# Kernel optimization log

Hardware: AMD Instinct MI355X
Metric: run time of the kernel (lower is better)

The kernel has to match this reference:

```python
import jax, jax.numpy as jnp
import numpy as np


def _layernorm(x, g, b, eps=1e-5):
    mu = jnp.mean(x, axis=-1, keepdims=True)
    xc = x - mu
    var = jnp.mean(xc * xc, axis=-1, keepdims=True)
    return xc * jax.lax.rsqrt(var + eps) * g + b


def _s5(u, Lambda_re, Lambda_im, B_re, B_im, C_re, C_im, Dskip, log_step):
    # Diagonal complex SSM with ZOH discretization (S5).
    Lam = Lambda_re + 1j * Lambda_im                       # (P,) complex64
    Lam_bar = jnp.exp(Lam * jnp.exp(log_step))             # (P,)
    B_bar = ((Lam_bar - 1.0) / Lam)[:, None] * (B_re + 1j * B_im)  # (P, D)
    Bu = jnp.einsum('bld,pd->blp', u.astype(jnp.complex64), B_bar)  # (B, L, P)
    A = jnp.broadcast_to(Lam_bar, Bu.shape)

    def combine(e1, e2):
        a1, b1 = e1
        a2, b2 = e2
        return a1 * a2, a2 * b1 + b2

    _, xs = jax.lax.associative_scan(combine, (A, Bu), axis=1)  # parallel scan over L
    y = 2.0 * jnp.real(jnp.einsum('blp,dp->bld', xs, C_re + 1j * C_im))
    return y + Dskip * u


def setup_inputs() -> dict:
    key = jax.random.key(0)
    ks = jax.random.split(key, 10)
    B, L, D, P = 4, 2048, 1024, 64
    F = int(D * 2.0)  # ff_mult = 2.0
    x = jax.random.normal(ks[0], (B, L, D), jnp.float32)
    ln1_g = jnp.ones((D,), jnp.float32)
    ln1_b = jnp.zeros((D,), jnp.float32)
    ln2_g = jnp.ones((D,), jnp.float32)
    ln2_b = jnp.zeros((D,), jnp.float32)
    Lambda_re = -(0.5 + jax.random.uniform(ks[1], (P,), jnp.float32))  # stable poles
    Lambda_im = jnp.pi * jnp.arange(P, dtype=jnp.float32)              # HiPPO-like spread
    B_re = jax.random.normal(ks[2], (P, D), jnp.float32) / np.float32(np.sqrt(D))
    B_im = jax.random.normal(ks[3], (P, D), jnp.float32) / np.float32(np.sqrt(D))
    C_re = jax.random.normal(ks[4], (D, P), jnp.float32) / np.float32(np.sqrt(P))
    C_im = jax.random.normal(ks[5], (D, P), jnp.float32) / np.float32(np.sqrt(P))
    Dskip = jax.random.normal(ks[6], (D,), jnp.float32)
    dt_min, dt_max = 1e-3, 1e-1
    log_step = (np.float32(np.log(dt_min))
                + jax.random.uniform(ks[7], (P,), jnp.float32)
                * np.float32(np.log(dt_max) - np.log(dt_min)))
    W_enc = jax.random.normal(ks[8], (2 * F, D), jnp.float32) / np.float32(np.sqrt(D))
    W_dec = jax.random.normal(ks[9], (D, F), jnp.float32) / np.float32(np.sqrt(F))
    return dict(x=x, ln1_g=ln1_g, ln1_b=ln1_b, ln2_g=ln2_g, ln2_b=ln2_b,
                Lambda_re=Lambda_re, Lambda_im=Lambda_im, B_re=B_re, B_im=B_im,
                C_re=C_re, C_im=C_im, Dskip=Dskip, log_step=log_step,
                W_enc=W_enc, W_dec=W_dec)


def reference(x, ln1_g, ln1_b, ln2_g, ln2_b, Lambda_re, Lambda_im, B_re, B_im,
              C_re, C_im, Dskip, log_step, W_enc, W_dec):
    # S5Block: pre-LN -> S5 -> GELU -> residual (dropout = identity in eval)
    fx = _layernorm(x, ln1_g, ln1_b)
    h = jax.nn.gelu(_s5(fx, Lambda_re, Lambda_im, B_re, B_im, C_re, C_im, Dskip, log_step),
                    approximate=False) + fx
    # pre-LN GEGLU feed-forward -> residual
    fx2 = _layernorm(h, ln2_g, ln2_b)
    e = fx2 @ W_enc.T                      # (B, L, 2F)
    a, gate = jnp.split(e, 2, axis=-1)
    e = a * jax.nn.gelu(gate, approximate=False)
    return e @ W_dec.T + fx2
```

## Files before the change

kernel.cpp:

```cpp
#include <hip/hip_runtime.h>
#include <hip/hip_bf16.h>
#include <math.h>

typedef unsigned short u16;
typedef __bf16 v8bf __attribute__((ext_vector_type(8)));
typedef float f32x4 __attribute__((ext_vector_type(4)));
typedef float f32x16 __attribute__((ext_vector_type(16)));

__device__ __forceinline__ float us2f(u16 h) {
    union { unsigned int u; float f; } v; v.u = ((unsigned int)h) << 16; return v.f;
}
__device__ __forceinline__ u16 f2us(float f) {
    union { float f; unsigned int u; } v; v.f = f;
    unsigned int r = v.u + 0x7fffu + ((v.u >> 16) & 1u);
    return (u16)(r >> 16);
}
__device__ __forceinline__ float gelu_f(float x) {
    return 0.5f * x * (1.0f + erff(x * 0.70710678118654752f));
}
__device__ __forceinline__ void gload_lds16(const u16* g, u16* l) {
    auto gp = reinterpret_cast<const __attribute__((address_space(1))) unsigned int*>(
        (uintptr_t)g);
    auto lp = reinterpret_cast<__attribute__((address_space(3))) unsigned int*>(
        (uintptr_t)l);
    __builtin_amdgcn_global_load_lds(gp, lp, 16, 0, 0);
}

__global__ __launch_bounds__(256) void prepall_kernel(
    const float* __restrict__ Wenc, u16* __restrict__ WeB,
    const float* __restrict__ Wdec, u16* __restrict__ WdB,
    const float* __restrict__ Lre, const float* __restrict__ Lim,
    const float* __restrict__ lstep,
    const float* __restrict__ Bre, const float* __restrict__ Bim,
    const float* __restrict__ Cre, const float* __restrict__ Cim,
    u16* __restrict__ Bbar, u16* __restrict__ C2)
{
    const int b = blockIdx.x, tid = threadIdx.x;
    if (b < 3072) {
        const float* in = (b < 2048) ? Wenc : Wdec;
        u16* outp = (b < 2048) ? WeB : WdB;
        const int i = (b < 2048 ? b : b - 2048) * 2048 + tid * 8;
        float4 a = *reinterpret_cast<const float4*>(in + i);
        float4 c = *reinterpret_cast<const float4*>(in + i + 4);
        u16 o[8] = { f2us(a.x), f2us(a.y), f2us(a.z), f2us(a.w),
                     f2us(c.x), f2us(c.y), f2us(c.z), f2us(c.w) };
        *reinterpret_cast<uint4*>(outp + i) = *reinterpret_cast<uint4*>(o);
        return;
    }
    const int idx = (b - 3072) * 256 + tid;
    if (idx < 65536) {
        const int p = idx >> 10, d = idx & 1023;
        const float lr = Lre[p], li = Lim[p];
        const float dt = expf(lstep[p]);
        const float er = expf(lr * dt);
        const float ar = er * cosf(li * dt), ai = er * sinf(li * dt);
        const float nr = ar - 1.0f, ni = ai;
        const float den = lr * lr + li * li;
        const float cr = (nr * lr + ni * li) / den;
        const float ci = (ni * lr - nr * li) / den;
        const float br = Bre[idx], bi = Bim[idx];
        Bbar[p * 1024 + d]        = f2us(cr * br - ci * bi);
        Bbar[(64 + p) * 1024 + d] = f2us(cr * bi + ci * br);
    } else {
        const int i = idx - 65536;
        const int d = i >> 6, p = i & 63;
        C2[d * 128 + p]      = f2us( 2.0f * Cre[i]);
        C2[d * 128 + 64 + p] = f2us(-2.0f * Cim[i]);
    }
}

template<typename TIN>
__global__ __launch_bounds__(256) void ln_kernel(const TIN* __restrict__ in,
                                                 const float* __restrict__ g,
                                                 const float* __restrict__ b,
                                                 u16* __restrict__ out)
{
    const int row = blockIdx.x, tid = threadIdx.x;
    const size_t base = (size_t)row * 1024 + tid * 4;
    float x0, x1, x2, x3;
    if constexpr (sizeof(TIN) == 4) {
        float4 v = *reinterpret_cast<const float4*>(in + base);
        x0 = v.x; x1 = v.y; x2 = v.z; x3 = v.w;
    } else {
        ushort4 v = *reinterpret_cast<const ushort4*>((const u16*)in + base);
        x0 = us2f(v.x); x1 = us2f(v.y); x2 = us2f(v.z); x3 = us2f(v.w);
    }
    float s = x0 + x1 + x2 + x3;
    float q = x0*x0 + x1*x1 + x2*x2 + x3*x3;
    #pragma unroll
    for (int o = 32; o; o >>= 1) { s += __shfl_down(s, o); q += __shfl_down(q, o); }
    __shared__ float red[8];
    if ((tid & 63) == 0) { red[tid >> 6] = s; red[4 + (tid >> 6)] = q; }
    __syncthreads();
    s = red[0] + red[1] + red[2] + red[3];
    q = red[4] + red[5] + red[6] + red[7];
    const float mu = s * (1.0f / 1024.0f);
    const float rs = rsqrtf(q * (1.0f / 1024.0f) - mu * mu + 1e-5f);
    float4 gv = *reinterpret_cast<const float4*>(g + tid * 4);
    float4 bv = *reinterpret_cast<const float4*>(b + tid * 4);
    ushort4 o4;
    o4.x = f2us((x0 - mu) * rs * gv.x + bv.x);
    o4.y = f2us((x1 - mu) * rs * gv.y + bv.y);
    o4.z = f2us((x2 - mu) * rs * gv.z + bv.z);
    o4.w = f2us((x3 - mu) * rs * gv.w + bv.w);
    *reinterpret_cast<ushort4*>(out + base) = o4;
}

__global__ __launch_bounds__(256) void scan_kernel(
    const float* __restrict__ Bu,
    const float* __restrict__ Lre, const float* __restrict__ Lim,
    const float* __restrict__ lstep,
    u16* __restrict__ A2)
{
    const int b = blockIdx.x >> 6;
    const int p = blockIdx.x & 63;
    const int t = threadIdx.x;
    const float lr = Lre[p], li = Lim[p];
    const float dt = expf(lstep[p]);
    const float er = expf(lr * dt);
    const float ar = er * cosf(li * dt), ai = er * sinf(li * dt);

    const size_t base = ((size_t)b * 2048 + t * 8) * 128;
    float xr[8], xi[8];
    float sr = 0.f, si = 0.f;
    #pragma unroll
    for (int i = 0; i < 8; ++i) {
        const float br = Bu[base + i * 128 + p];
        const float bi = Bu[base + i * 128 + 64 + p];
        const float nr = ar * sr - ai * si + br;
        const float ni = ar * si + ai * sr + bi;
        sr = nr; si = ni;
        xr[i] = sr; xi[i] = si;
    }
    float fr = ar, fi = ai;
    #pragma unroll
    for (int s = 0; s < 3; ++s) { const float t2 = fr*fr - fi*fi; fi = 2.f*fr*fi; fr = t2; }
    __shared__ float Er[256], Ei[256];
    Er[t] = sr; Ei[t] = si;
    __syncthreads();
    float vr = sr, vi = si;
    for (int off = 1; off < 256; off <<= 1) {
        float pr = 0.f, pi = 0.f;
        if (t >= off) { pr = Er[t - off]; pi = Ei[t - off]; }
        __syncthreads();
        vr += fr * pr - fi * pi;
        vi += fr * pi + fi * pr;
        Er[t] = vr; Ei[t] = vi;
        const float nf = fr*fr - fi*fi; fi = 2.f*fr*fi; fr = nf;
        __syncthreads();
    }
    float cr = 0.f, ci = 0.f;
    if (t > 0) { cr = Er[t - 1]; ci = Ei[t - 1]; }
    float gr = ar * cr - ai * ci, gi = ar * ci + ai * cr;
    #pragma unroll
    for (int i = 0; i < 8; ++i) {
        xr[i] += gr; xi[i] += gi;
        const float n2 = ar * gr - ai * gi; gi = ar * gi + ai * gr; gr = n2;
    }
    #pragma unroll
    for (int i = 0; i < 8; ++i) {
        const size_t m = (size_t)b * 2048 + t * 8 + i;
        A2[m * 128 + p]      = f2us(xr[i]);
        A2[m * 128 + 64 + p] = f2us(xi[i]);
    }
}

template<int BM, int BN>
__global__ __launch_bounds__(64) void gemm_small_kernel(
    const u16* __restrict__ A, const u16* __restrict__ B, float* __restrict__ Cout,
    const int N, const int K)
{
    __shared__ u16 lsA[BM * 32];
    __shared__ u16 lsB[BN * 32];
    const int tid = threadIdx.x;
    const int lane = tid & 63;
    const int m0 = blockIdx.y * BM, n0 = blockIdx.x * BN;
    f32x4 acc[4][4] = {};
    for (int k0 = 0; k0 < K; k0 += 32) {
        #pragma unroll
        for (int j = 0; j < 4; ++j) {
            const int s = j * 64 + tid;
            gload_lds16(A + (size_t)(m0 + (s >> 2)) * K + k0 + (s & 3) * 8,
                        lsA + (s - lane) * 8);
            gload_lds16(B + (size_t)(n0 + (s >> 2)) * K + k0 + (s & 3) * 8,
                        lsB + (s - lane) * 8);
        }
        __syncthreads();
        v8bf af[4], bfv[4];
        #pragma unroll
        for (int f = 0; f < 4; ++f)
            af[f] = *reinterpret_cast<const v8bf*>(
                lsA + (f * 16 + (lane & 15)) * 32 + (lane >> 4) * 8);
        #pragma unroll
        for (int f = 0; f < 4; ++f)
            bfv[f] = *reinterpret_cast<const v8bf*>(
                lsB + (f * 16 + (lane & 15)) * 32 + (lane >> 4) * 8);
        #pragma unroll
        for (int fm = 0; fm < 4; ++fm)
            #pragma unroll
            for (int fn = 0; fn < 4; ++fn)
                acc[fm][fn] = __builtin_amdgcn_mfma_f32_16x16x32_bf16(
                    af[fm], bfv[fn], acc[fm][fn], 0, 0, 0);
        __syncthreads();
    }
    #pragma unroll
    for (int fm = 0; fm < 4; ++fm)
    #pragma unroll
    for (int fn = 0; fn < 4; ++fn)
    #pragma unroll
    for (int i = 0; i < 4; ++i) {
        const int r = m0 + fm * 16 + (lane >> 4) * 4 + i;
        const int c = n0 + fn * 16 + (lane & 15);
        Cout[(size_t)r * N + c] = acc[fm][fn][i];
    }
}

#define BARM()   asm volatile("s_barrier" ::: "memory")
#define LGKM0()  asm volatile("s_waitcnt lgkmcnt(0)" ::: "memory")
#define VMK(n)   asm volatile("s_waitcnt vmcnt(" #n ")" ::: "memory")
#define PRIO1    __builtin_amdgcn_s_setprio(1)
#define PRIO0    __builtin_amdgcn_s_setprio(0)
#define MMA32(acc, a, b) \
    acc = __builtin_amdgcn_mfma_f32_32x32x16_bf16(a, b, acc, 0, 0, 0)
#define RDA(mf, kk) (*reinterpret_cast<const v8bf*>( \
    cb + ((wm) * 128 + (mf) * 32 + l31) * 64 + ((((kk) * 2 + lh) ^ l7) * 8)))
#define RDBG(ag, kk) (*reinterpret_cast<const v8bf*>( \
    cb + (256 + (ag) * 128 + (wn) * 32 + l31) * 64 + ((((kk) * 2 + lh) ^ l7) * 8)))
#define RDB4(kk) (*reinterpret_cast<const v8bf*>( \
    cb + (256 + (wn) * 32 + l31) * 64 + ((((kk) * 2 + lh) ^ l7) * 8)))
#define STAGE(s, bi) do { \
    u16* d0_ = lds + (bi) * BUFE + ((s) * 128 + (wid * 2 + 0) * 8) * 64; \
    u16* d1_ = lds + (bi) * BUFE + ((s) * 128 + (wid * 2 + 1) * 8) * 64; \
    gload_lds16(pS[s][0], d0_); gload_lds16(pS[s][1], d1_); \
    pS[s][0] += 64; pS[s][1] += 64; } while (0)

#define GLU_HB(cb_, ab_, bb_, stA_, stB_) do { \
    const u16* cb = (cb_); \
    v8bf bfA[4], bfG[4], af[4]; \
    _Pragma("unroll") for (int mf = 0; mf < 4; ++mf) af[mf] = RDA(mf, 0); \
    _Pragma("unroll") for (int kk = 0; kk < 4; ++kk) { \
        bfA[kk] = RDBG(0, kk); bfG[kk] = RDBG(1, kk); } \
    if (stA_) STAGE(0, ab_); \
    PRIO1; \
    _Pragma("unroll") for (int mf = 0; mf < 4; ++mf) { \
        MMA32(accA[mf], af[mf], bfA[0]); MMA32(accG[mf], af[mf], bfG[0]); } \
    PRIO0; LGKM0(); BARM(); \
    _Pragma("unroll") for (int mf = 0; mf < 4; ++mf) af[mf] = RDA(mf, 1); \
    if (stA_) STAGE(1, ab_); \
    PRIO1; \
    _Pragma("unroll") for (int mf = 0; mf < 4; ++mf) { \
        MMA32(accA[mf], af[mf], bfA[1]); MMA32(accG[mf], af[mf], bfG[1]); } \
    PRIO0; LGKM0(); BARM(); \
    _Pragma("unroll") for (int mf = 0; mf < 4; ++mf) af[mf] = RDA(mf, 2); \
    if (stB_) STAGE(2, bb_); \
    PRIO1; \
    _Pragma("unroll") for (int mf = 0; mf < 4; ++mf) { \
        MMA32(accA[mf], af[mf], bfA[2]); MMA32(accG[mf], af[mf], bfG[2]); } \
    PRIO0; LGKM0(); BARM(); \
    _Pragma("unroll") for (int mf = 0; mf < 4; ++mf) af[mf] = RDA(mf, 3); \
    if (stB_) STAGE(3, bb_); \
    PRIO1; \
    _Pragma("unroll") for (int mf = 0; mf < 4; ++mf) { \
        MMA32(accA[mf], af[mf], bfA[3]); MMA32(accG[mf], af[mf], bfG[3]); } \
    PRIO0; LGKM0(); \
    if (stB_) { VMK(4); } else { VMK(0); } \
    BARM(); } while (0)

template<int NBX>
__global__ __launch_bounds__(512, 2) void geglu8p_kernel(
    const u16* __restrict__ A, const u16* __restrict__ Bm, u16* __restrict__ Cout,
    const int K, const int NO, const int NT)
{
    constexpr int BUFE = 512 * 64;
    __shared__ u16 lds[2 * BUFE];
    const int tid = threadIdx.x, lane = tid & 63, wid = tid >> 6;
    const int wm = wid >> 2, wn = wid & 3;
    const int l31 = lane & 31, lh = lane >> 5, l7 = lane & 7;
    const int bid = blockIdx.x;
    const int swz = (bid & 7) * (NBX * 4) + (bid >> 3);
    const int by = swz / NBX, bx = swz % NBX;
    const int m0 = by * 256, n0 = bx * 128;

    const int rl = lane >> 3;
    const int scol = ((lane & 7) ^ rl) * 8;
    const u16* pS[4][2];
    #pragma unroll
    for (int j = 0; j < 2; ++j) {
        const int rloc = (wid * 2 + j) * 8 + rl;
        pS[0][j] = A  + (size_t)(m0 + rloc)       * K + scol;
        pS[1][j] = A  + (size_t)(m0 + 128 + rloc) * K + scol;
        pS[2][j] = Bm + (size_t)(n0 + rloc)       * K + scol;
        pS[3][j] = Bm + (size_t)(NO + n0 + rloc)  * K + scol;
    }

    f32x16 accA[4] = {};
    f32x16 accG[4] = {};

    #pragma unroll
    for (int t = 0; t < 2; ++t) { STAGE(0, t); STAGE(1, t); STAGE(2, t); STAGE(3, t); }
    VMK(0);
    BARM();

    const int NI = NT >> 1;
    for (int i = 0; i < NI; ++i) {
        const bool s1 = (i > 0);
        const bool s2 = (2 * i + 2 < NT);
        const bool s3 = (2 * i + 3 < NT);
        GLU_HB(lds,        1, 0, s1, s2);
        GLU_HB(lds + BUFE, 0, 1, s2, s3);
    }

    #pragma unroll
    for (int mf = 0; mf < 4; ++mf)
    #pragma unroll
    for (int q = 0; q < 16; ++q) {
        const int r = m0 + wm * 128 + mf * 32 + (q & 3) + 8 * (q >> 2) + 4 * lh;
        const int c = n0 + wn * 32 + l31;
        Cout[(size_t)r * NO + c] = f2us(accA[mf][q] * gelu_f(accG[mf][q]));
    }
}

#define P4_HB(cb_, ab_, bb_, stA_, stB_) do { \
    const u16* cb = (cb_); \
    v8bf bfv[4], af0[4], af1[4]; \
    _Pragma("unroll") for (int mf = 0; mf < 4; ++mf) { \
        af0[mf] = RDA(mf, 0); af1[mf] = RDA(mf, 1); } \
    _Pragma("unroll") for (int kk = 0; kk < 4; ++kk) bfv[kk] = RDB4(kk); \
    if (stA_) { STAGE(0, ab_); STAGE(1, ab_); } \
    PRIO1; \
    _Pragma("unroll") for (int mf = 0; mf < 4; ++mf) { \
        MMA32(acc[mf], af0[mf], bfv[0]); MMA32(acc[mf], af1[mf], bfv[1]); } \
    PRIO0; LGKM0(); BARM(); \
    _Pragma("unroll") for (int mf = 0; mf < 4; ++mf) { \
        af0[mf] = RDA(mf, 2); af1[mf] = RDA(mf, 3); } \
    if (stB_) STAGE(2, bb_); \
    PRIO1; \
    _Pragma("unroll") for (int mf = 0; mf < 4; ++mf) { \
        MMA32(acc[mf], af0[mf], bfv[2]); MMA32(acc[mf], af1[mf], bfv[3]); } \
    PRIO0; LGKM0(); \
    if (stB_) { VMK(2); } else { VMK(0); } \
    BARM(); } while (0)

template<int EPI, int NBX>
__global__ __launch_bounds__(512, 2) void gemm4p_kernel(
    const u16* __restrict__ A, const u16* __restrict__ Bm, void* __restrict__ Cout,
    const int K, const int NO, const int NT,
    const u16* __restrict__ aux, const float* __restrict__ dskip)
{
    constexpr int BUFE = 384 * 64;
    __shared__ u16 lds[2 * BUFE];
    const int tid = threadIdx.x, lane = tid & 63, wid = tid >> 6;
    const int wm = wid >> 2, wn = wid & 3;
    const int l31 = lane & 31, lh = lane >> 5, l7 = lane & 7;
    const int bid = blockIdx.x;
    const int swz = (bid & 7) * (NBX * 4) + (bid >> 3);
    const int by = swz / NBX, bx = swz % NBX;
    const int m0 = by * 256, n0 = bx * 128;

    const int rl = lane >> 3;
    const int scol = ((lane & 7) ^ rl) * 8;
    const u16* pS[3][2];
    #pragma unroll
    for (int j = 0; j < 2; ++j) {
        const int rloc = (wid * 2 + j) * 8 + rl;
        pS[0][j] = A  + (size_t)(m0 + rloc)       * K + scol;
        pS[1][j] = A  + (size_t)(m0 + 128 + rloc) * K + scol;
        pS[2][j] = Bm + (size_t)(n0 + rloc)       * K + scol;
    }

    f32x16 acc[4] = {};

    #pragma unroll
    for (int t = 0; t < 2; ++t) { STAGE(0, t); STAGE(1, t); STAGE(2, t); }
    VMK(0);
    BARM();

    const int NI = NT >> 1;
    for (int i = 0; i < NI; ++i) {
        const bool s1 = (i > 0);
        const bool s2 = (2 * i + 2 < NT);
        const bool s3 = (2 * i + 3 < NT);
        P4_HB(lds,        1, 0, s1, s2);
        P4_HB(lds + BUFE, 0, 1, s2, s3);
    }

    #pragma unroll
    for (int mf = 0; mf < 4; ++mf)
    #pragma unroll
    for (int q = 0; q < 16; ++q) {
        const int r = m0 + wm * 128 + mf * 32 + (q & 3) + 8 * (q >> 2) + 4 * lh;
        const int c = n0 + wn * 32 + l31;
        const size_t o = (size_t)r * NO + c;
        const float v = acc[mf][q];
        if constexpr (EPI == 1) {
            const float u = us2f(aux[o]);
            const float t2 = v + dskip[c] * u;
            ((u16*)Cout)[o] = f2us(gelu_f(t2) + u);
        } else {
            ((float*)Cout)[o] = v + us2f(aux[o]);
        }
    }
}

static constexpr size_t OFF_FX  = 0;
static constexpr size_t OFF_BU  = 16777216;
static constexpr size_t OFF_A2  = 20971520;
static constexpr size_t OFF_E2  = 0;
static constexpr size_t OFF_FX2 = 33554432;
static constexpr size_t OFF_BB  = 50331648;
static constexpr size_t OFF_C2  = 50593792;
static constexpr size_t OFF_WE  = 50855936;
static constexpr size_t OFF_WD  = 59244544;

extern "C" void kernel_launch(void* const* d_in, const int* in_sizes, int n_in,
                              void* d_out, int out_size, void* d_ws, size_t ws_size,
                              hipStream_t stream) {
    const float* x    = (const float*)d_in[0];
    const float* l1g  = (const float*)d_in[1];
    const float* l1b  = (const float*)d_in[2];
    const float* l2g  = (const float*)d_in[3];
    const float* l2b  = (const float*)d_in[4];
    const float* Lre  = (const float*)d_in[5];
    const float* Lim  = (const float*)d_in[6];
    const float* Bre  = (const float*)d_in[7];
    const float* Bim  = (const float*)d_in[8];
    const float* Cre  = (const float*)d_in[9];
    const float* Cim  = (const float*)d_in[10];
    const float* Dsk  = (const float*)d_in[11];
    const float* lst  = (const float*)d_in[12];
    const float* Wenc = (const float*)d_in[13];
    const float* Wdec = (const float*)d_in[14];
    float* out = (float*)d_out;

    char* ws = (char*)d_ws;
    u16*   fx   = (u16*)(ws + OFF_FX);
    float* Bu   = (float*)(ws + OFF_BU);
    u16*   A2   = (u16*)(ws + OFF_A2);
    u16*   e2   = (u16*)(ws + OFF_E2);
    u16*   fx2  = (u16*)(ws + OFF_FX2);
    u16*   Bbar = (u16*)(ws + OFF_BB);
    u16*   C2   = (u16*)(ws + OFF_C2);
    u16*   WeB  = (u16*)(ws + OFF_WE);
    u16*   WdB  = (u16*)(ws + OFF_WD);
    u16*   h    = (u16*)d_out;

    ln_kernel<float><<<8192, 256, 0, stream>>>(x, l1g, l1b, fx);
    prepall_kernel<<<3584, 256, 0, stream>>>(Wenc, WeB, Wdec, WdB,
                                             Lre, Lim, lst, Bre, Bim, Cre, Cim,
                                             Bbar, C2);
    gemm_small_kernel<64, 64><<<dim3(2, 128), 64, 0, stream>>>(
        fx, Bbar, Bu, 128, 1024);
    scan_kernel<<<256, 256, 0, stream>>>(Bu, Lre, Lim, lst, A2);
    gemm4p_kernel<1, 8><<<256, 512, 0, stream>>>(
        A2, C2, h, 128, 1024, 2, fx, Dsk);
    ln_kernel<u16><<<8192, 256, 0, stream>>>(h, l2g, l2b, fx2);
    geglu8p_kernel<16><<<512, 512, 0, stream>>>(fx2, WeB, e2, 1024, 2048, 16);
    gemm4p_kernel<3, 8><<<256, 512, 0, stream>>>(
        e2, WdB, out, 2048, 1024, 32, fx2, nullptr);

    (void)in_sizes; (void)n_in; (void)out_size; (void)ws_size;
}
```

Before: 230.4 us.

## Retile down/C-projection GEMMs to 128x128 with 256-thread blocks, precompute LDS pointers

The 4-pass GEMM kernel (used for the S5 C-projection and the GEGLU down projection) moves from 256x128 tiles with 512 threads to 128x128 tiles with 256 threads and a 2x2 warp grid, each warp computing 64x64. The grid doubles to 512 blocks to improve CU occupancy and load balance. The GEGLU kernel keeps its tiling but gets a new LDS layout with A and B regions separated and per-lane LDS read pointers precomputed, which cuts address arithmetic. Smaller tiles lower per-block reuse and raise total global traffic, in exchange for more parallelism.

```diff
diff --git a/kernel.cpp b/kernel.cpp
--- a/kernel.cpp
+++ b/kernel.cpp
@@ -222,62 +222,51 @@
 #define PRIO0    __builtin_amdgcn_s_setprio(0)
 #define MMA32(acc, a, b) \
     acc = __builtin_amdgcn_mfma_f32_32x32x16_bf16(a, b, acc, 0, 0, 0)
-#define RDA(mf, kk) (*reinterpret_cast<const v8bf*>( \
-    cb + ((wm) * 128 + (mf) * 32 + l31) * 64 + ((((kk) * 2 + lh) ^ l7) * 8)))
-#define RDBG(ag, kk) (*reinterpret_cast<const v8bf*>( \
-    cb + (256 + (ag) * 128 + (wn) * 32 + l31) * 64 + ((((kk) * 2 + lh) ^ l7) * 8)))
-#define RDB4(kk) (*reinterpret_cast<const v8bf*>( \
-    cb + (256 + (wn) * 32 + l31) * 64 + ((((kk) * 2 + lh) ^ l7) * 8)))
-#define STAGE(s, bi) do { \
-    u16* d0_ = lds + (bi) * BUFE + ((s) * 128 + (wid * 2 + 0) * 8) * 64; \
-    u16* d1_ = lds + (bi) * BUFE + ((s) * 128 + (wid * 2 + 1) * 8) * 64; \
-    gload_lds16(pS[s][0], d0_); gload_lds16(pS[s][1], d1_); \
+
+#define G_RA(af, kk, BI) { _Pragma("unroll") \
+    for (int mf = 0; mf < 4; ++mf) \
+        af[mf] = *reinterpret_cast<const v8bf*>(pA[kk] + mf * 2048 + (BI) * 16384); }
+#define G_RB(kk, ag, BI) \
+    (*reinterpret_cast<const v8bf*>(pB[kk] + (ag) * 8192 + (BI) * 16384))
+#define G_ST(s, bi) do { \
+    const int db_ = (((s) & 2) ? 32768 : 0) + (bi) * 16384 + (((s) & 1) ? 8192 : 0); \
+    gload_lds16(pS[s][0], lds + db_ + (wid * 2 + 0) * 512); \
+    gload_lds16(pS[s][1], lds + db_ + (wid * 2 + 1) * 512); \
     pS[s][0] += 64; pS[s][1] += 64; } while (0)
-
-#define GLU_HB(cb_, ab_, bb_, stA_, stB_) do { \
-    const u16* cb = (cb_); \
-    v8bf bfA[4], bfG[4], af[4]; \
-    _Pragma("unroll") for (int mf = 0; mf < 4; ++mf) af[mf] = RDA(mf, 0); \
+#define G_MM(kk) { _Pragma("unroll") \
+    for (int mf = 0; mf < 4; ++mf) { \
+        MMA32(accA[mf], af[mf], bA[kk]); MMA32(accG[mf], af[mf], bG[kk]); } }
+#define G_TILE(BI, stA_, stB_) do { \
+    v8bf af[4], bA[4], bG[4]; \
+    G_RA(af, 0, BI); \
     _Pragma("unroll") for (int kk = 0; kk < 4; ++kk) { \
-        bfA[kk] = RDBG(0, kk); bfG[kk] = RDBG(1, kk); } \
-    if (stA_) STAGE(0, ab_); \
-    PRIO1; \
-    _Pragma("unroll") for (int mf = 0; mf < 4; ++mf) { \
-        MMA32(accA[mf], af[mf], bfA[0]); MMA32(accG[mf], af[mf], bfG[0]); } \
-    PRIO0; LGKM0(); BARM(); \
-    _Pragma("unroll") for (int mf = 0; mf < 4; ++mf) af[mf] = RDA(mf, 1); \
-    if (stA_) STAGE(1, ab_); \
-    PRIO1; \
-    _Pragma("unroll") for (int mf = 0; mf < 4; ++mf) { \
-        MMA32(accA[mf], af[mf], bfA[1]); MMA32(accG[mf], af[mf], bfG[1]); } \
-    PRIO0; LGKM0(); BARM(); \
-    _Pragma("unroll") for (int mf = 0; mf < 4; ++mf) af[mf] = RDA(mf, 2); \
-    if (stB_) STAGE(2, bb_); \
-    PRIO1; \
-    _Pragma("unroll") for (int mf = 0; mf < 4; ++mf) { \
-        MMA32(accA[mf], af[mf], bfA[2]); MMA32(accG[mf], af[mf], bfG[2]); } \
-    PRIO0; LGKM0(); BARM(); \
-    _Pragma("unroll") for (int mf = 0; mf < 4; ++mf) af[mf] = RDA(mf, 3); \
-    if (stB_) STAGE(3, bb_); \
-    PRIO1; \
-    _Pragma("unroll") for (int mf = 0; mf < 4; ++mf) { \
-        MMA32(accA[mf], af[mf], bfA[3]); MMA32(accG[mf], af[mf], bfG[3]); } \
-    PRIO0; LGKM0(); \
+        bA[kk] = G_RB(kk, 0, BI); bG[kk] = G_RB(kk, 1, BI); } \
+    if (stA_) G_ST(0, (BI) ^ 1); \
+    PRIO1; G_MM(0); PRIO0; LGKM0(); BARM(); \
+    G_RA(af, 1, BI); \
+    if (stA_) G_ST(1, (BI) ^ 1); \
+    PRIO1; G_MM(1); PRIO0; LGKM0(); BARM(); \
+    G_RA(af, 2, BI); \
+    if (stB_) G_ST(2, BI); \
+    PRIO1; G_MM(2); PRIO0; LGKM0(); BARM(); \
+    G_RA(af, 3, BI); \
+    if (stB_) G_ST(3, BI); \
+    PRIO1; G_MM(3); PRIO0; LGKM0(); \
     if (stB_) { VMK(4); } else { VMK(0); } \
     BARM(); } while (0)
 
 template<int NBX>
-__global__ __launch_bounds__(512, 2) void geglu8p_kernel(
+__global__ __launch_bounds__(512, 2) void geglu_kernel(
     const u16* __restrict__ A, const u16* __restrict__ Bm, u16* __restrict__ Cout,
     const int K, const int NO, const int NT)
 {
-    constexpr int BUFE = 512 * 64;
-    __shared__ u16 lds[2 * BUFE];
+    __shared__ u16 lds[65536];
     const int tid = threadIdx.x, lane = tid & 63, wid = tid >> 6;
     const int wm = wid >> 2, wn = wid & 3;
     const int l31 = lane & 31, lh = lane >> 5, l7 = lane & 7;
     const int bid = blockIdx.x;
-    const int swz = (bid & 7) * (NBX * 4) + (bid >> 3);
+    const int chunk = (int)gridDim.x >> 3;
+    const int swz = (bid & 7) * chunk + (bid >> 3);
     const int by = swz / NBX, bx = swz % NBX;
     const int m0 = by * 256, n0 = bx * 128;
 
@@ -292,12 +281,20 @@
         pS[2][j] = Bm + (size_t)(n0 + rloc)       * K + scol;
         pS[3][j] = Bm + (size_t)(NO + n0 + rloc)  * K + scol;
     }
+    const u16* pA[4];
+    const u16* pB[4];
+    #pragma unroll
+    for (int kk = 0; kk < 4; ++kk) {
+        const int phys = ((kk * 2 + lh) ^ l7) * 8;
+        pA[kk] = lds + (wm * 128 + l31) * 64 + phys;
+        pB[kk] = lds + 32768 + (wn * 32 + l31) * 64 + phys;
+    }
 
     f32x16 accA[4] = {};
     f32x16 accG[4] = {};
 
     #pragma unroll
-    for (int t = 0; t < 2; ++t) { STAGE(0, t); STAGE(1, t); STAGE(2, t); STAGE(3, t); }
+    for (int t = 0; t < 2; ++t) { G_ST(0, t); G_ST(1, t); G_ST(2, t); G_ST(3, t); }
     VMK(0);
     BARM();
 
@@ -306,8 +303,8 @@
         const bool s1 = (i > 0);
         const bool s2 = (2 * i + 2 < NT);
         const bool s3 = (2 * i + 3 < NT);
-        GLU_HB(lds,        1, 0, s1, s2);
-        GLU_HB(lds + BUFE, 0, 1, s2, s3);
+        G_TILE(0, s1, s2);
+        G_TILE(1, s2, s3);
     }
 
     #pragma unroll
@@ -320,58 +317,80 @@
     }
 }
 
-#define P4_HB(cb_, ab_, bb_, stA_, stB_) do { \
-    const u16* cb = (cb_); \
-    v8bf bfv[4], af0[4], af1[4]; \
-    _Pragma("unroll") for (int mf = 0; mf < 4; ++mf) { \
-        af0[mf] = RDA(mf, 0); af1[mf] = RDA(mf, 1); } \
-    _Pragma("unroll") for (int kk = 0; kk < 4; ++kk) bfv[kk] = RDB4(kk); \
-    if (stA_) { STAGE(0, ab_); STAGE(1, ab_); } \
+#define Q_RA2(af, k0_, BI) { _Pragma("unroll") \
+    for (int mf = 0; mf < 2; ++mf) _Pragma("unroll") \
+    for (int kq = 0; kq < 2; ++kq) \
+        af[mf][kq] = *reinterpret_cast<const v8bf*>( \
+            qA[(k0_) + kq] + mf * 2048 + (BI) * 8192); }
+#define Q_ST(s, bi) do { \
+    const int db_ = ((s) >= 4 ? 16384 : 0) + (bi) * 8192 + ((s) & 3) * 2048; \
+    gload_lds16(qS[s], lds + db_ + wid * 512); qS[s] += 64; } while (0)
+#define Q_TILE(BI, stA_, stB_) do { \
+    v8bf af[2][2], bf[2][4]; \
+    Q_RA2(af, 0, BI); \
+    _Pragma("unroll") for (int cf = 0; cf < 2; ++cf) _Pragma("unroll") \
+    for (int kk = 0; kk < 4; ++kk) \
+        bf[cf][kk] = *reinterpret_cast<const v8bf*>( \
+            qB[kk] + cf * 2048 + (BI) * 8192); \
+    if (stA_) { Q_ST(0, (BI) ^ 1); Q_ST(1, (BI) ^ 1); Q_ST(2, (BI) ^ 1); Q_ST(3, (BI) ^ 1); } \
     PRIO1; \
-    _Pragma("unroll") for (int mf = 0; mf < 4; ++mf) { \
-        MMA32(acc[mf], af0[mf], bfv[0]); MMA32(acc[mf], af1[mf], bfv[1]); } \
+    _Pragma("unroll") for (int mf = 0; mf < 2; ++mf) _Pragma("unroll") \
+    for (int cf = 0; cf < 2; ++cf) { \
+        MMA32(acc[mf][cf], af[mf][0], bf[cf][0]); \
+        MMA32(acc[mf][cf], af[mf][1], bf[cf][1]); } \
     PRIO0; LGKM0(); BARM(); \
-    _Pragma("unroll") for (int mf = 0; mf < 4; ++mf) { \
-        af0[mf] = RDA(mf, 2); af1[mf] = RDA(mf, 3); } \
-    if (stB_) STAGE(2, bb_); \
+    Q_RA2(af, 2, BI); \
+    if (stB_) { Q_ST(4, BI); Q_ST(5, BI); Q_ST(6, BI); Q_ST(7, BI); } \
     PRIO1; \
-    _Pragma("unroll") for (int mf = 0; mf < 4; ++mf) { \
-        MMA32(acc[mf], af0[mf], bfv[2]); MMA32(acc[mf], af1[mf], bfv[3]); } \
+    _Pragma("unroll") for (int mf = 0; mf < 2; ++mf) _Pragma("unroll") \
+    for (int cf = 0; cf < 2; ++cf) { \
+        MMA32(acc[mf][cf], af[mf][0], bf[cf][2]); \
+        MMA32(acc[mf][cf], af[mf][1], bf[cf][3]); } \
     PRIO0; LGKM0(); \
-    if (stB_) { VMK(2); } else { VMK(0); } \
+    if (stB_) { VMK(4); } else { VMK(0); } \
     BARM(); } while (0)
 
 template<int EPI, int NBX>
-__global__ __launch_bounds__(512, 2) void gemm4p_kernel(
+__global__ __launch_bounds__(256, 2) void gemm4p_kernel(
     const u16* __restrict__ A, const u16* __restrict__ Bm, void* __restrict__ Cout,
     const int K, const int NO, const int NT,
     const u16* __restrict__ aux, const float* __restrict__ dskip)
 {
-    constexpr int BUFE = 384 * 64;
-    __shared__ u16 lds[2 * BUFE];
+    __shared__ u16 lds[32768];
     const int tid = threadIdx.x, lane = tid & 63, wid = tid >> 6;
-    const int wm = wid >> 2, wn = wid & 3;
+    const int wm = wid >> 1, wn = wid & 1;
     const int l31 = lane & 31, lh = lane >> 5, l7 = lane & 7;
     const int bid = blockIdx.x;
-    const int swz = (bid & 7) * (NBX * 4) + (bid >> 3);
+    const int chunk = (int)gridDim.x >> 3;
+    const int swz = (bid & 7) * chunk + (bid >> 3);
     const int by = swz / NBX, bx = swz % NBX;
-    const int m0 = by * 256, n0 = bx * 128;
+    const int m0 = by * 128, n0 = bx * 128;
 
     const int rl = lane >> 3;
     const int scol = ((lane & 7) ^ rl) * 8;
-    const u16* pS[3][2];
-    #pragma unroll
-    for (int j = 0; j < 2; ++j) {
-        const int rloc = (wid * 2 + j) * 8 + rl;
-        pS[0][j] = A  + (size_t)(m0 + rloc)       * K + scol;
-        pS[1][j] = A  + (size_t)(m0 + 128 + rloc) * K + scol;
-        pS[2][j] = Bm + (size_t)(n0 + rloc)       * K + scol;
-    }
-
-    f32x16 acc[4] = {};
-
-    #pragma unroll
-    for (int t = 0; t < 2; ++t) { STAGE(0, t); STAGE(1, t); STAGE(2, t); }
+    const u16* qS[8];
+    #pragma unroll
+    for (int s = 0; s < 4; ++s)
+        qS[s] = A + (size_t)(m0 + s * 32 + wid * 8 + rl) * K + scol;
+    #pragma unroll
+    for (int s = 4; s < 8; ++s)
+        qS[s] = Bm + (size_t)(n0 + (s - 4) * 32 + wid * 8 + rl) * K + scol;
+    const u16* qA[4];
+    const u16* qB[4];
+    #pragma unroll
+    for (int kk = 0; kk < 4; ++kk) {
+        const int phys = ((kk * 2 + lh) ^ l7) * 8;
+        qA[kk] = lds + (wm * 64 + l31) * 64 + phys;
+        qB[kk] = lds + 16384 + (wn * 64 + l31) * 64 + phys;
+    }
+
+    f32x16 acc[2][2] = {};
+
+    #pragma unroll
+    for (int t = 0; t < 2; ++t) {
+        Q_ST(0, t); Q_ST(1, t); Q_ST(2, t); Q_ST(3, t);
+        Q_ST(4, t); Q_ST(5, t); Q_ST(6, t); Q_ST(7, t);
+    }
     VMK(0);
     BARM();
 
@@ -380,18 +399,20 @@
         const bool s1 = (i > 0);
         const bool s2 = (2 * i + 2 < NT);
         const bool s3 = (2 * i + 3 < NT);
-        P4_HB(lds,        1, 0, s1, s2);
-        P4_HB(lds + BUFE, 0, 1, s2, s3);
-    }
-
-    #pragma unroll
-    for (int mf = 0; mf < 4; ++mf)
+        Q_TILE(0, s1, s2);
+        Q_TILE(1, s2, s3);
+    }
+
+    #pragma unroll
+    for (int mf = 0; mf < 2; ++mf)
+    #pragma unroll
+    for (int cf = 0; cf < 2; ++cf)
     #pragma unroll
     for (int q = 0; q < 16; ++q) {
-        const int r = m0 + wm * 128 + mf * 32 + (q & 3) + 8 * (q >> 2) + 4 * lh;
-        const int c = n0 + wn * 32 + l31;
+        const int r = m0 + wm * 64 + mf * 32 + (q & 3) + 8 * (q >> 2) + 4 * lh;
+        const int c = n0 + wn * 64 + cf * 32 + l31;
         const size_t o = (size_t)r * NO + c;
-        const float v = acc[mf][q];
+        const float v = acc[mf][cf][q];
         if constexpr (EPI == 1) {
             const float u = us2f(aux[o]);
             const float t2 = v + dskip[c] * u;
@@ -451,11 +472,11 @@
     gemm_small_kernel<64, 64><<<dim3(2, 128), 64, 0, stream>>>(
         fx, Bbar, Bu, 128, 1024);
     scan_kernel<<<256, 256, 0, stream>>>(Bu, Lre, Lim, lst, A2);
-    gemm4p_kernel<1, 8><<<256, 512, 0, stream>>>(
+    gemm4p_kernel<1, 8><<<512, 256, 0, stream>>>(
         A2, C2, h, 128, 1024, 2, fx, Dsk);
     ln_kernel<u16><<<8192, 256, 0, stream>>>(h, l2g, l2b, fx2);
-    geglu8p_kernel<16><<<512, 512, 0, stream>>>(fx2, WeB, e2, 1024, 2048, 16);
-    gemm4p_kernel<3, 8><<<256, 512, 0, stream>>>(
+    geglu_kernel<16><<<512, 512, 0, stream>>>(fx2, WeB, e2, 1024, 2048, 16);
+    gemm4p_kernel<3, 8><<<512, 256, 0, stream>>>(
         e2, WdB, out, 2048, 1024, 32, fx2, nullptr);
 
     (void)in_sizes; (void)n_in; (void)out_size; (void)ws_size;
```

Result: faster. 223.4 us (-3.1%).
